# Kernel optimization log

Hardware: AMD Instinct MI355X
Metric: run time of the kernel (lower is better)

## Reference

```python
import jax, jax.numpy as jnp
import numpy as np

B, C, H, W = 32, 64, 32, 32
DIM = H * W          # number of tokens (pixels)
DEPTH = 8
TAU = 1.0
NUM_CLASSES = 10


def setup_inputs() -> dict:
    key = jax.random.key(0)
    ks = jax.random.split(key, 6)
    return {
        "image": jax.random.normal(ks[0], (B, C, H, W), dtype=jnp.float32),
        "WV": 10.0 * jax.random.normal(ks[1], (C, C), dtype=jnp.float32),
        "WK": jax.random.normal(ks[2], (C, C), dtype=jnp.float32),
        "WQ": jax.random.normal(ks[3], (C, C), dtype=jnp.float32),
        "last_W": jax.random.normal(ks[4], (NUM_CLASSES, DIM), dtype=jnp.float32) / np.sqrt(DIM),
        "last_b": jnp.zeros((NUM_CLASSES,), dtype=jnp.float32),
    }


def reference(image, WV, WK, WQ, last_W, last_b):
    # flatten(2).transpose(1,2): (B,C,H,W) -> (B, H*W, C)
    X = image.reshape(B, C, DIM).transpose(0, 2, 1)
    scale = DIM ** (-0.5)
    for _ in range(DEPTH):
        # weight_sharing=True, sign=0 -> W = WV every layer
        Q = X @ WQ                                  # (B, n, C)
        K = X @ WK                                  # (B, n, C)
        scores = jnp.einsum('bnc,bmc->bnm', Q, K) * scale  # (B, n, n)
        A = jax.nn.softmax(scores, axis=-1)
        # diffusion_step (method 'A'): tau * A @ (X @ W) + X
        X = TAU * jnp.einsum('bnm,bmc->bnc', A, X @ WV) + X
    # mean over channel dim -> (B, dim), then Linear(dim, num_classes)
    pred = X.mean(-1) @ last_W.T + last_b
    return pred
```

## Files before the change

### kernel.cpp

```cpp
#include <hip/hip_runtime.h>
#include <math.h>

#define BB    32
#define CCH   64
#define DIMN  1024
#define NCLS  10

typedef __attribute__((ext_vector_type(8))) short bf16x8;
typedef __attribute__((ext_vector_type(4))) float f32x4;
typedef __attribute__((ext_vector_type(4))) unsigned short us4;
typedef __attribute__((ext_vector_type(8))) unsigned short us8;

#define MFMA16(a, b, c) __builtin_amdgcn_mfma_f32_16x16x32_bf16(a, b, c, 0, 0, 0)

__device__ __forceinline__ unsigned short f2bf(float x) {
  unsigned u = __float_as_uint(x);
  unsigned r = u + 0x7fffu + ((u >> 16) & 1u);
  return (unsigned short)(r >> 16);
}
__device__ __forceinline__ float bf2f(unsigned short h) {
  return __uint_as_float(((unsigned)h) << 16);
}
__device__ __forceinline__ void split3_pk(float x0, float x1,
                                          unsigned& hp, unsigned& mp,
                                          unsigned& lp) {
  unsigned h, m, l;
  asm("v_cvt_pk_bf16_f32 %0, %1, %2" : "=v"(h) : "v"(x0), "v"(x1));
  const float h0 = __uint_as_float(h << 16);
  const float h1 = __uint_as_float(h & 0xffff0000u);
  const float r0 = x0 - h0, r1 = x1 - h1;
  asm("v_cvt_pk_bf16_f32 %0, %1, %2" : "=v"(m) : "v"(r0), "v"(r1));
  const float m0 = __uint_as_float(m << 16);
  const float m1 = __uint_as_float(m & 0xffff0000u);
  asm("v_cvt_pk_bf16_f32 %0, %1, %2" : "=v"(l) : "v"(r0 - m0), "v"(r1 - m1));
  hp = h; mp = m; lp = l;
}
__device__ __forceinline__ void split3_pk2(float x0, float x1,
    unsigned short& h0, unsigned short& m0, unsigned short& l0,
    unsigned short& h1, unsigned short& m1, unsigned short& l1) {
  unsigned h, m, l;
  split3_pk(x0, x1, h, m, l);
  h0 = (unsigned short)h; h1 = (unsigned short)(h >> 16);
  m0 = (unsigned short)m; m1 = (unsigned short)(m >> 16);
  l0 = (unsigned short)l; l1 = (unsigned short)(l >> 16);
}
__device__ __forceinline__ void split3_frag(const float* xv, bf16x8& fh,
                                            bf16x8& fm, bf16x8& fl) {
  union U { bf16x8 v; unsigned d[4]; } uh, um, ul;
  #pragma unroll
  for (int p = 0; p < 4; ++p)
    split3_pk(xv[2 * p], xv[2 * p + 1], uh.d[p], um.d[p], ul.d[p]);
  fh = uh.v; fm = um.v; fl = ul.v;
}
__device__ __forceinline__ bf16x8 ld16B(const unsigned short* p) {
  union { us8 u; bf16x8 v; } c;
  c.u = *(const us8*)p;
  return c.v;
}

__global__ __launch_bounds__(256) void k_transpose(const float* __restrict__ img,
                                                   float* __restrict__ X) {
  __shared__ float tile[64][65];
  const int b  = blockIdx.y;
  const int n0 = blockIdx.x * 64;
  const int tx = threadIdx.x & 63;
  const int ty = threadIdx.x >> 6;
  const float* src = img + (size_t)b * CCH * DIMN;
  #pragma unroll
  for (int c = ty; c < 64; c += 4)
    tile[c][tx] = src[(size_t)c * DIMN + n0 + tx];
  __syncthreads();
  float* dst = X + (size_t)b * DIMN * CCH;
  #pragma unroll
  for (int nn = ty; nn < 64; nn += 4)
    dst[(size_t)(n0 + nn) * CCH + tx] = tile[tx][nn];
}

__device__ __forceinline__ void qkv_inner(
    const float xs[16][64],
    const float* __restrict__ WQ, const float* __restrict__ WK,
    const float* __restrict__ WV, int c, int tg,
    float qa[4], float ka[4], float va[4]) {
  for (int j = 0; j < 64; j += 4) {
    float4 xv[4];
    #pragma unroll
    for (int r = 0; r < 4; ++r)
      xv[r] = *(const float4*)&xs[tg * 4 + r][j];
    #pragma unroll
    for (int jj = 0; jj < 4; ++jj) {
      const float wq = WQ[(j + jj) * 64 + c];
      const float wk = WK[(j + jj) * 64 + c];
      const float wv = WV[(j + jj) * 64 + c];
      #pragma unroll
      for (int r = 0; r < 4; ++r) {
        const float x = ((const float*)&xv[r])[jj];
        qa[r] = fmaf(x, wq, qa[r]);
        ka[r] = fmaf(x, wk, ka[r]);
        va[r] = fmaf(x, wv, va[r]);
      }
    }
  }
}

__global__ __launch_bounds__(256) void k_qkv_split(
    const float* __restrict__ X,
    const float* __restrict__ WQ, const float* __restrict__ WK,
    const float* __restrict__ WV,
    float* __restrict__ Q,
    unsigned short* __restrict__ Kh, unsigned short* __restrict__ Km,
    unsigned short* __restrict__ Kl,
    unsigned short* __restrict__ VhT, unsigned short* __restrict__ VmT,
    unsigned short* __restrict__ VlT) {
  __shared__ float xs[16][64];
  __shared__ unsigned short vs[3][16][64];
  const int c  = threadIdx.x & 63;
  const int tg = threadIdx.x >> 6;
  const size_t t0 = (size_t)blockIdx.x * 16;
  #pragma unroll
  for (int r = tg; r < 16; r += 4)
    xs[r][c] = X[(t0 + r) * 64 + c];
  __syncthreads();
  float qa[4] = {0.f,0.f,0.f,0.f};
  float ka[4] = {0.f,0.f,0.f,0.f};
  float va[4] = {0.f,0.f,0.f,0.f};
  qkv_inner(xs, WQ, WK, WV, c, tg, qa, ka, va);
  #pragma unroll
  for (int pr = 0; pr < 2; ++pr) {
    const int r0 = 2 * pr, r1 = 2 * pr + 1;
    const int ta = tg * 4 + r0, tb = tg * 4 + r1;
    const size_t ia = (t0 + ta) * 64 + c;
    const size_t ib = (t0 + tb) * 64 + c;
    Q[ia] = qa[r0]; Q[ib] = qa[r1];
    unsigned short h0, m0, l0, h1, m1, l1;
    split3_pk2(ka[r0], ka[r1], h0, m0, l0, h1, m1, l1);
    Kh[ia] = h0; Km[ia] = m0; Kl[ia] = l0;
    Kh[ib] = h1; Km[ib] = m1; Kl[ib] = l1;
    split3_pk2(va[r0], va[r1], h0, m0, l0, h1, m1, l1);
    vs[0][ta][c] = h0; vs[1][ta][c] = m0; vs[2][ta][c] = l0;
    vs[0][tb][c] = h1; vs[1][tb][c] = m1; vs[2][tb][c] = l1;
  }
  __syncthreads();
  {
    const int row  = threadIdx.x >> 2;
    const int part = threadIdx.x & 3;
    const size_t bofs = (t0 >> 10) * ((size_t)DIMN * 64);
    const size_t kt   = (t0 & 1023) >> 5;
    const size_t tin  = (size_t)part * 8 + ((t0 & 31) >> 2);
    unsigned short* dst[3] = {VhT, VmT, VlT};
    #pragma unroll
    for (int term = 0; term < 3; ++term) {
      us4 pk;
      #pragma unroll
      for (int i = 0; i < 4; ++i) pk[i] = vs[term][part * 4 + i][row];
      *(us4*)&dst[term][bofs + kt * 2048 + (size_t)row * 32 + tin] = pk;
    }
  }
}

__global__ __launch_bounds__(256) void k_qkv_merge(
    float* __restrict__ X,
    const float* __restrict__ Mp, const float* __restrict__ Lp,
    const float* __restrict__ Op,
    const float* __restrict__ WQ, const float* __restrict__ WK,
    const float* __restrict__ WV,
    float* __restrict__ Q,
    unsigned short* __restrict__ Kh, unsigned short* __restrict__ Km,
    unsigned short* __restrict__ Kl,
    unsigned short* __restrict__ VhT, unsigned short* __restrict__ VmT,
    unsigned short* __restrict__ VlT) {
  __shared__ float xs[16][64];
  __shared__ unsigned short vs[3][16][64];
  const int c  = threadIdx.x & 63;
  const int tg = threadIdx.x >> 6;
  const size_t t0 = (size_t)blockIdx.x * 16;
  #pragma unroll
  for (int r = tg; r < 16; r += 4) {
    const size_t grow = t0 + r;
    const float m0 = Mp[grow], m1 = Mp[32768 + grow];
    const float l0 = Lp[grow], l1 = Lp[32768 + grow];
    const float mm = fmaxf(m0, m1);
    const float w0 = __expf(m0 - mm), w1 = __expf(m1 - mm);
    const float inv = 1.0f / (l0 * w0 + l1 * w1);
    const float o0 = Op[grow * 64 + c];
    const float o1 = Op[(size_t)2097152 + grow * 64 + c];
    const float xn = X[grow * 64 + c] + (o0 * w0 + o1 * w1) * inv;
    X[grow * 64 + c] = xn;
    xs[r][c] = xn;
  }
  __syncthreads();
  float qa[4] = {0.f,0.f,0.f,0.f};
  float ka[4] = {0.f,0.f,0.f,0.f};
  float va[4] = {0.f,0.f,0.f,0.f};
  qkv_inner(xs, WQ, WK, WV, c, tg, qa, ka, va);
  #pragma unroll
  for (int pr = 0; pr < 2; ++pr) {
    const int r0 = 2 * pr, r1 = 2 * pr + 1;
    const int ta = tg * 4 + r0, tb = tg * 4 + r1;
    const size_t ia = (t0 + ta) * 64 + c;
    const size_t ib = (t0 + tb) * 64 + c;
    Q[ia] = qa[r0]; Q[ib] = qa[r1];
    unsigned short h0, m0, l0, h1, m1, l1;
    split3_pk2(ka[r0], ka[r1], h0, m0, l0, h1, m1, l1);
    Kh[ia] = h0; Km[ia] = m0; Kl[ia] = l0;
    Kh[ib] = h1; Km[ib] = m1; Kl[ib] = l1;
    split3_pk2(va[r0], va[r1], h0, m0, l0, h1, m1, l1);
    vs[0][ta][c] = h0; vs[1][ta][c] = m0; vs[2][ta][c] = l0;
    vs[0][tb][c] = h1; vs[1][tb][c] = m1; vs[2][tb][c] = l1;
  }
  __syncthreads();
  {
    const int row  = threadIdx.x >> 2;
    const int part = threadIdx.x & 3;
    const size_t bofs = (t0 >> 10) * ((size_t)DIMN * 64);
    const size_t kt   = (t0 & 1023) >> 5;
    const size_t tin  = (size_t)part * 8 + ((t0 & 31) >> 2);
    unsigned short* dst[3] = {VhT, VmT, VlT};
    #pragma unroll
    for (int term = 0; term < 3; ++term) {
      us4 pk;
      #pragma unroll
      for (int i = 0; i < 4; ++i) pk[i] = vs[term][part * 4 + i][row];
      *(us4*)&dst[term][bofs + kt * 2048 + (size_t)row * 32 + tin] = pk;
    }
  }
}

__global__ __launch_bounds__(256, 2) void k_attn_sk(
    const float* __restrict__ Qg,
    const unsigned short* __restrict__ Kh, const unsigned short* __restrict__ Km,
    const unsigned short* __restrict__ Kl,
    const unsigned short* __restrict__ VhT, const unsigned short* __restrict__ VmT,
    const unsigned short* __restrict__ VlT,
    float* __restrict__ Mp, float* __restrict__ Lp, float* __restrict__ Op) {
  __shared__ __align__(16) unsigned short Khs[32 * 72];
  __shared__ __align__(16) unsigned short Kms[32 * 72];
  __shared__ __align__(16) unsigned short Kls[32 * 72];
  __shared__ __align__(16) unsigned short Vhs[64 * 40];
  __shared__ __align__(16) unsigned short Vms[64 * 40];
  __shared__ __align__(16) unsigned short Vls[64 * 40];

  const int tid  = threadIdx.x;
  const int w    = tid >> 6;
  const int lane = tid & 63;
  const int ln   = lane & 15;
  const int q    = lane >> 4;

  const int bid   = blockIdx.x;
  const int xcd   = bid & 7;
  const int seq   = bid >> 3;
  const int b     = xcd * 4 + (seq >> 4);
  const int local = seq & 15;
  const int half  = local >> 3;
  const int i0    = (local & 7) * 128;

  const size_t base = (size_t)b * (DIMN * 64);
  const float scale = 0.03125f;

  const int kj = tid >> 3, kg = tid & 7;
  const int vc = tid >> 2, vg = tid & 3;
  const int klo = kj * 72 + kg * 8;
  const int vlo = vc * 40 + vg * 8;

  bf16x8 qh[2][2], qm[2][2], ql[2][2];
  #pragma unroll
  for (int t = 0; t < 2; ++t) {
    const int mrow = i0 + 64 * t + 16 * w + ln;
    const float* qp = Qg + base + (size_t)mrow * 64 + 8 * q;
    #pragma unroll
    for (int s = 0; s < 2; ++s) {
      const float4 x0 = ((const float4*)(qp + 32 * s))[0];
      const float4 x1 = ((const float4*)(qp + 32 * s))[1];
      const float xv[8] = {x0.x, x0.y, x0.z, x0.w, x1.x, x1.y, x1.z, x1.w};
      split3_frag(xv, qh[t][s], qm[t][s], ql[t][s]);
    }
  }

  f32x4 O[2][4];
  #pragma unroll
  for (int t = 0; t < 2; ++t)
    #pragma unroll
    for (int ct = 0; ct < 4; ++ct) O[t][ct] = (f32x4){0.f, 0.f, 0.f, 0.f};
  float m_run[2] = {-INFINITY, -INFINITY};
  float l_run[2] = {0.f, 0.f};

  const int kt0 = half * 16;
  for (int kt = kt0; kt < kt0 + 16; ++kt) {
    __syncthreads();

    {
      const size_t tof = base + (size_t)kt * 2048 + tid * 8;
      const us8 a0 = *(const us8*)&Kh[tof];
      const us8 a1 = *(const us8*)&Km[tof];
      const us8 a2 = *(const us8*)&Kl[tof];
      const us8 b0 = *(const us8*)&VhT[tof];
      const us8 b1 = *(const us8*)&VmT[tof];
      const us8 b2 = *(const us8*)&VlT[tof];
      *(us8*)&Khs[klo] = a0;
      *(us8*)&Kms[klo] = a1;
      *(us8*)&Kls[klo] = a2;
      *(us8*)&Vhs[vlo] = b0;
      *(us8*)&Vms[vlo] = b1;
      *(us8*)&Vls[vlo] = b2;
    }
    __syncthreads();

    f32x4 sacc[2][2];
    __builtin_amdgcn_s_setprio(1);
    #pragma unroll
    for (int ct = 0; ct < 2; ++ct) {
      f32x4 aA = (f32x4){0.f, 0.f, 0.f, 0.f};
      f32x4 aB = (f32x4){0.f, 0.f, 0.f, 0.f};
      #pragma unroll
      for (int s = 0; s < 2; ++s) {
        const int ko = (16 * ct + ln) * 72 + 32 * s + 8 * q;
        const bf16x8 bh = ld16B(&Khs[ko]);
        const bf16x8 bm = ld16B(&Kms[ko]);
        const bf16x8 bl = ld16B(&Kls[ko]);
        aA = MFMA16(bh, ql[0][s], aA);
        aA = MFMA16(bl, qh[0][s], aA);
        aA = MFMA16(bm, qm[0][s], aA);
        aA = MFMA16(bh, qm[0][s], aA);
        aA = MFMA16(bm, qh[0][s], aA);
        aA = MFMA16(bh, qh[0][s], aA);
        aB = MFMA16(bh, ql[1][s], aB);
        aB = MFMA16(bl, qh[1][s], aB);
        aB = MFMA16(bm, qm[1][s], aB);
        aB = MFMA16(bh, qm[1][s], aB);
        aB = MFMA16(bm, qh[1][s], aB);
        aB = MFMA16(bh, qh[1][s], aB);
      }
      sacc[0][ct] = aA; sacc[1][ct] = aB;
    }
    __builtin_amdgcn_s_setprio(0);

    bf16x8 ph[2], pm[2], pl[2];
    const int srcb = (lane & 48) + ((lane & 48) >> 2);
    #pragma unroll
    for (int t = 0; t < 2; ++t) {
      float m8 = fmaxf(fmaxf(fmaxf(sacc[t][0][0], sacc[t][0][1]),
                             fmaxf(sacc[t][0][2], sacc[t][0][3])),
                       fmaxf(fmaxf(sacc[t][1][0], sacc[t][1][1]),
                             fmaxf(sacc[t][1][2], sacc[t][1][3])));
      m8 = fmaxf(m8, __shfl_xor(m8, 16, 64));
      m8 = fmaxf(m8, __shfl_xor(m8, 32, 64));
      const float mnew  = fmaxf(m_run[t], m8 * scale);
      const float alpha = __expf(m_run[t] - mnew);
      m_run[t] = mnew;

      float pv[8];
      float s8 = 0.f;
      #pragma unroll
      for (int ct = 0; ct < 2; ++ct) {
        #pragma unroll
        for (int r = 0; r < 4; ++r) {
          const float p = __expf(sacc[t][ct][r] * scale - m_run[t]);
          pv[ct * 4 + r] = p;
          s8 += p;
        }
      }
      float sr = s8 + __shfl_xor(s8, 16, 64);
      sr = sr + __shfl_xor(sr, 32, 64);
      l_run[t] = l_run[t] * alpha + sr;

      float arow[4];
      #pragma unroll
      for (int r = 0; r < 4; ++r) arow[r] = __shfl(alpha, srcb + r, 64);
      #pragma unroll
      for (int ct = 0; ct < 4; ++ct) {
        #pragma unroll
        for (int r = 0; r < 4; ++r) O[t][ct][r] *= arow[r];
      }

      split3_frag(pv, ph[t], pm[t], pl[t]);
    }

    __builtin_amdgcn_s_setprio(1);
    #pragma unroll
    for (int ct = 0; ct < 4; ++ct) {
      const int vo = (16 * ct + ln) * 40 + 8 * q;
      const bf16x8 vvh = ld16B(&Vhs[vo]);
      const bf16x8 vvm = ld16B(&Vms[vo]);
      const bf16x8 vvl = ld16B(&Vls[vo]);
      O[0][ct] = MFMA16(ph[0], vvh, O[0][ct]);
      O[0][ct] = MFMA16(ph[0], vvm, O[0][ct]);
      O[0][ct] = MFMA16(pm[0], vvh, O[0][ct]);
      O[0][ct] = MFMA16(pm[0], vvm, O[0][ct]);
      O[0][ct] = MFMA16(ph[0], vvl, O[0][ct]);
      O[0][ct] = MFMA16(pl[0], vvh, O[0][ct]);
      O[1][ct] = MFMA16(ph[1], vvh, O[1][ct]);
      O[1][ct] = MFMA16(ph[1], vvm, O[1][ct]);
      O[1][ct] = MFMA16(pm[1], vvh, O[1][ct]);
      O[1][ct] = MFMA16(pm[1], vvm, O[1][ct]);
      O[1][ct] = MFMA16(ph[1], vvl, O[1][ct]);
      O[1][ct] = MFMA16(pl[1], vvh, O[1][ct]);
    }
    __builtin_amdgcn_s_setprio(0);
  }

  const size_t hofs = (size_t)half * (32 * 1024);
  #pragma unroll
  for (int t = 0; t < 2; ++t) {
    const int ti0 = i0 + 64 * t;
    #pragma unroll
    for (int r = 0; r < 4; ++r) {
      const int row = ti0 + 16 * w + 4 * q + r;
      const size_t grow = hofs + (size_t)b * DIMN + row;
      #pragma unroll
      for (int ct = 0; ct < 4; ++ct)
        Op[grow * 64 + ln + 16 * ct] = O[t][ct][r];
    }
    if (q == 0) {
      const size_t tgrow = hofs + (size_t)b * DIMN + ti0 + 16 * w + ln;
      Mp[tgrow] = m_run[t];
      Lp[tgrow] = l_run[t];
    }
  }
}

__global__ __launch_bounds__(256) void k_merge_mean(
    const float* __restrict__ X,
    const float* __restrict__ Mp, const float* __restrict__ Lp,
    const float* __restrict__ Op, float* __restrict__ meanv) {
  const int c  = threadIdx.x & 63;
  const int tg = threadIdx.x >> 6;
  const size_t t0 = (size_t)blockIdx.x * 128;
  for (int i = tg; i < 128; i += 4) {
    const size_t grow = t0 + i;
    const float m0 = Mp[grow], m1 = Mp[32768 + grow];
    const float l0 = Lp[grow], l1 = Lp[32768 + grow];
    const float mm = fmaxf(m0, m1);
    const float w0 = __expf(m0 - mm), w1 = __expf(m1 - mm);
    const float inv = 1.0f / (l0 * w0 + l1 * w1);
    const float o0 = Op[grow * 64 + c];
    const float o1 = Op[(size_t)2097152 + grow * 64 + c];
    float v = X[grow * 64 + c] + (o0 * w0 + o1 * w1) * inv;
    #pragma unroll
    for (int off = 32; off > 0; off >>= 1)
      v += __shfl_down(v, off, 64);
    if (c == 0) meanv[grow] = v * (1.0f / 64.0f);
  }
}

__global__ __launch_bounds__(256) void k_head2(
    const float* __restrict__ meanv, const float* __restrict__ lW,
    const float* __restrict__ lb, float* __restrict__ out) {
  __shared__ float red[256];
  const int b   = blockIdx.x;
  const int tid = threadIdx.x;
  float acc[NCLS];
  #pragma unroll
  for (int k = 0; k < NCLS; ++k) acc[k] = 0.f;
  for (int n = tid; n < DIMN; n += 256) {
    const float m = meanv[(size_t)b * DIMN + n];
    #pragma unroll
    for (int k = 0; k < NCLS; ++k)
      acc[k] = fmaf(m, lW[k * DIMN + n], acc[k]);
  }
  for (int k = 0; k < NCLS; ++k) {
    red[tid] = acc[k];
    __syncthreads();
    for (int s = 128; s > 0; s >>= 1) {
      if (tid < s) red[tid] += red[tid + s];
      __syncthreads();
    }
    if (tid == 0) out[b * NCLS + k] = red[0] + lb[k];
    __syncthreads();
  }
}

__global__ __launch_bounds__(256) void k_attn_s(
    const float* __restrict__ Qg,
    const unsigned short* __restrict__ Kh, const unsigned short* __restrict__ Km,
    const unsigned short* __restrict__ Kl,
    const unsigned short* __restrict__ VhT, const unsigned short* __restrict__ VmT,
    const unsigned short* __restrict__ VlT,
    float* __restrict__ X, float* __restrict__ meanout) {
  __shared__ __align__(16) unsigned short Khs[32 * 72];
  __shared__ __align__(16) unsigned short Kms[32 * 72];
  __shared__ __align__(16) unsigned short Kls[32 * 72];
  __shared__ __align__(16) unsigned short Vhs[64 * 40];
  __shared__ __align__(16) unsigned short Vms[64 * 40];
  __shared__ __align__(16) unsigned short Vls[64 * 40];

  const int tid  = threadIdx.x;
  const int w    = tid >> 6;
  const int lane = tid & 63;
  const int ln   = lane & 15;
  const int q    = lane >> 4;
  const int bid = blockIdx.x;
  const int xcd = bid & 7;
  const int seq = bid >> 3;
  const int b   = xcd * 4 + (seq >> 4);
  const int i0  = (seq & 15) * 64;
  const size_t base = (size_t)b * (DIMN * 64);
  const float scale = 0.03125f;

  const int kj = tid >> 3, kg = tid & 7;
  const int vc = tid >> 2, vg = tid & 3;
  const int klo = kj * 72 + kg * 8;
  const int vlo = vc * 40 + vg * 8;

  bf16x8 qh[2], qm[2], ql[2];
  {
    const int mrow = i0 + 16 * w + ln;
    const float* qp = Qg + base + (size_t)mrow * 64 + 8 * q;
    #pragma unroll
    for (int s = 0; s < 2; ++s) {
      const float4 x0 = ((const float4*)(qp + 32 * s))[0];
      const float4 x1 = ((const float4*)(qp + 32 * s))[1];
      const float xv[8] = {x0.x, x0.y, x0.z, x0.w, x1.x, x1.y, x1.z, x1.w};
      split3_frag(xv, qh[s], qm[s], ql[s]);
    }
  }

  f32x4 O[4];
  #pragma unroll
  for (int ct = 0; ct < 4; ++ct) O[ct] = (f32x4){0.f, 0.f, 0.f, 0.f};
  float m_run = -INFINITY;
  float l_run = 0.f;

  for (int kt = 0; kt < 32; ++kt) {
    __syncthreads();
    {
      const size_t tof = base + (size_t)kt * 2048 + tid * 8;
      const us8 a0 = *(const us8*)&Kh[tof];
      const us8 a1 = *(const us8*)&Km[tof];
      const us8 a2 = *(const us8*)&Kl[tof];
      const us8 b0 = *(const us8*)&VhT[tof];
      const us8 b1 = *(const us8*)&VmT[tof];
      const us8 b2 = *(const us8*)&VlT[tof];
      *(us8*)&Khs[klo] = a0;
      *(us8*)&Kms[klo] = a1;
      *(us8*)&Kls[klo] = a2;
      *(us8*)&Vhs[vlo] = b0;
      *(us8*)&Vms[vlo] = b1;
      *(us8*)&Vls[vlo] = b2;
    }
    __syncthreads();

    f32x4 sacc[2];
    #pragma unroll
    for (int ct = 0; ct < 2; ++ct) {
      f32x4 a = (f32x4){0.f, 0.f, 0.f, 0.f};
      #pragma unroll
      for (int s = 0; s < 2; ++s) {
        const int ko = (16 * ct + ln) * 72 + 32 * s + 8 * q;
        const bf16x8 bh = ld16B(&Khs[ko]);
        const bf16x8 bm = ld16B(&Kms[ko]);
        const bf16x8 bl = ld16B(&Kls[ko]);
        a = MFMA16(bh, ql[s], a);
        a = MFMA16(bl, qh[s], a);
        a = MFMA16(bm, qm[s], a);
        a = MFMA16(bh, qm[s], a);
        a = MFMA16(bm, qh[s], a);
        a = MFMA16(bh, qh[s], a);
      }
      sacc[ct] = a;
    }

    float m8 = fmaxf(fmaxf(fmaxf(sacc[0][0], sacc[0][1]),
                           fmaxf(sacc[0][2], sacc[0][3])),
                     fmaxf(fmaxf(sacc[1][0], sacc[1][1]),
                           fmaxf(sacc[1][2], sacc[1][3])));
    m8 = fmaxf(m8, __shfl_xor(m8, 16, 64));
    m8 = fmaxf(m8, __shfl_xor(m8, 32, 64));
    const float mnew  = fmaxf(m_run, m8 * scale);
    const float alpha = __expf(m_run - mnew);
    m_run = mnew;

    float pv[8];
    float s8 = 0.f;
    #pragma unroll
    for (int ct = 0; ct < 2; ++ct) {
      #pragma unroll
      for (int r = 0; r < 4; ++r) {
        const float p = __expf(sacc[ct][r] * scale - m_run);
        pv[ct * 4 + r] = p;
        s8 += p;
      }
    }
    float sr = s8 + __shfl_xor(s8, 16, 64);
    sr = sr + __shfl_xor(sr, 32, 64);
    l_run = l_run * alpha + sr;

    const int srcb = (lane & 48) + ((lane & 48) >> 2);
    float arow[4];
    #pragma unroll
    for (int r = 0; r < 4; ++r) arow[r] = __shfl(alpha, srcb + r, 64);
    #pragma unroll
    for (int ct = 0; ct < 4; ++ct) {
      #pragma unroll
      for (int r = 0; r < 4; ++r) O[ct][r] *= arow[r];
    }

    bf16x8 ph, pm, pl;
    split3_frag(pv, ph, pm, pl);

    #pragma unroll
    for (int ct = 0; ct < 4; ++ct) {
      const int vo = (16 * ct + ln) * 40 + 8 * q;
      const bf16x8 vvh = ld16B(&Vhs[vo]);
      const bf16x8 vvm = ld16B(&Vms[vo]);
      const bf16x8 vvl = ld16B(&Vls[vo]);
      O[ct] = MFMA16(ph, vvh, O[ct]);
      O[ct] = MFMA16(ph, vvm, O[ct]);
      O[ct] = MFMA16(pm, vvh, O[ct]);
      O[ct] = MFMA16(pm, vvm, O[ct]);
      O[ct] = MFMA16(ph, vvl, O[ct]);
      O[ct] = MFMA16(pl, vvh, O[ct]);
    }
  }

  const int srcb = (lane & 48) + ((lane & 48) >> 2);
  float linv[4];
  #pragma unroll
  for (int r = 0; r < 4; ++r) linv[r] = 1.0f / __shfl(l_run, srcb + r, 64);
  #pragma unroll
  for (int r = 0; r < 4; ++r) {
    const int row = i0 + 16 * w + 4 * q + r;
    float srow = 0.f;
    #pragma unroll
    for (int ct = 0; ct < 4; ++ct) {
      float* xp = X + base + (size_t)row * 64 + ln + 16 * ct;
      const float nv = *xp + O[ct][r] * linv[r];
      *xp = nv;
      srow += nv;
    }
    if (meanout) {
      #pragma unroll
      for (int mk = 1; mk <= 8; mk <<= 1)
        srow += __shfl_xor(srow, mk, 64);
      if (ln == 0) meanout[(size_t)b * DIMN + row] = srow * (1.0f / 64.0f);
    }
  }
}

extern "C" void kernel_launch(void* const* d_in, const int* in_sizes, int n_in,
                              void* d_out, int out_size, void* d_ws, size_t ws_size,
                              hipStream_t stream) {
  const float* image = (const float*)d_in[0];
  const float* WV    = (const float*)d_in[1];
  const float* WK    = (const float*)d_in[2];
  const float* WQ    = (const float*)d_in[3];
  const float* lW    = (const float*)d_in[4];
  const float* lb    = (const float*)d_in[5];
  float* out = (float*)d_out;

  float* ws = (float*)d_ws;
  const size_t NELEM = (size_t)BB * DIMN * CCH;
  const size_t NROW  = (size_t)BB * DIMN;

  const size_t need_sk   = (7 * NELEM + 5 * NROW) * sizeof(float);
  const size_t need_fast = (5 * NELEM + NROW) * sizeof(float);

  if (ws_size >= need_sk) {
    float* X = ws;
    float* Q = ws + NELEM;
    unsigned short* Kh  = (unsigned short*)(ws + 2 * NELEM);
    unsigned short* Km  = Kh + NELEM;
    unsigned short* Kl  = Kh + 2 * NELEM;
    unsigned short* VhT = Kh + 3 * NELEM;
    unsigned short* VmT = Kh + 4 * NELEM;
    unsigned short* VlT = Kh + 5 * NELEM;
    float* Op    = ws + 5 * NELEM;
    float* Mp    = ws + 7 * NELEM;
    float* Lp    = Mp + 2 * NROW;
    float* meanv = Lp + 2 * NROW;

    k_transpose<<<dim3(DIMN / 64, BB), 256, 0, stream>>>(image, X);
    k_qkv_split<<<(BB * DIMN) / 16, 256, 0, stream>>>(
        X, WQ, WK, WV, Q, Kh, Km, Kl, VhT, VmT, VlT);
    for (int layer = 0; layer < 8; ++layer) {
      k_attn_sk<<<512, 256, 0, stream>>>(
          Q, Kh, Km, Kl, VhT, VmT, VlT, Mp, Lp, Op);
      if (layer < 7)
        k_qkv_merge<<<(BB * DIMN) / 16, 256, 0, stream>>>(
            X, Mp, Lp, Op, WQ, WK, WV, Q, Kh, Km, Kl, VhT, VmT, VlT);
    }
    k_merge_mean<<<256, 256, 0, stream>>>(X, Mp, Lp, Op, meanv);
    k_head2<<<BB, 256, 0, stream>>>(meanv, lW, lb, out);
  } else {
    float* X = ws;
    float* Q = ws + NELEM;
    unsigned short* Kh  = (unsigned short*)(ws + 2 * NELEM);
    unsigned short* Km  = Kh + NELEM;
    unsigned short* Kl  = Kh + 2 * NELEM;
    unsigned short* VhT = Kh + 3 * NELEM;
    unsigned short* VmT = Kh + 4 * NELEM;
    unsigned short* VlT = Kh + 5 * NELEM;
    float* meanv = ws + 5 * NELEM;
    (void)need_fast;

    k_transpose<<<dim3(DIMN / 64, BB), 256, 0, stream>>>(image, X);
    for (int layer = 0; layer < 8; ++layer) {
      k_qkv_split<<<(BB * DIMN) / 16, 256, 0, stream>>>(
          X, WQ, WK, WV, Q, Kh, Km, Kl, VhT, VmT, VlT);
      k_attn_s<<<512, 256, 0, stream>>>(
          Q, Kh, Km, Kl, VhT, VmT, VlT, X, (layer == 7) ? meanv : nullptr);
    }
    k_head2<<<BB, 256, 0, stream>>>(meanv, lW, lb, out);
  }
}
```

Before: 700.9 us.

## Double-buffer K/V tiles in LDS with register prefetch in attention kernel

The attention kernel now keeps two LDS buffers for the K and V hi/mid/lo tiles. It issues the global loads for the next tile into registers before the MFMA compute on the current tile and writes them to the other buffer afterwards. This lets global memory latency overlap with compute and removes one barrier per iteration. LDS use doubles to about 58KB per block, which may limit the two-blocks-per-CU target, and the held registers raise register pressure.

Result: faster. 676.7 us (-3.4%).

```diff
diff --git a/kernel.cpp b/kernel.cpp
--- a/kernel.cpp
+++ b/kernel.cpp
@@ -232,12 +232,7 @@
     const unsigned short* __restrict__ VhT, const unsigned short* __restrict__ VmT,
     const unsigned short* __restrict__ VlT,
     float* __restrict__ Mp, float* __restrict__ Lp, float* __restrict__ Op) {
-  __shared__ __align__(16) unsigned short Khs[32 * 72];
-  __shared__ __align__(16) unsigned short Kms[32 * 72];
-  __shared__ __align__(16) unsigned short Kls[32 * 72];
-  __shared__ __align__(16) unsigned short Vhs[64 * 40];
-  __shared__ __align__(16) unsigned short Vms[64 * 40];
-  __shared__ __align__(16) unsigned short Vls[64 * 40];
+  __shared__ __align__(16) unsigned short lds[2][14592];
 
   const int tid  = threadIdx.x;
   const int w    = tid >> 6;
@@ -284,25 +279,47 @@
   float l_run[2] = {0.f, 0.f};
 
   const int kt0 = half * 16;
+
+  {
+    const size_t tof = base + (size_t)kt0 * 2048 + tid * 8;
+    const us8 a0 = *(const us8*)&Kh[tof];
+    const us8 a1 = *(const us8*)&Km[tof];
+    const us8 a2 = *(const us8*)&Kl[tof];
+    const us8 b0 = *(const us8*)&VhT[tof];
+    const us8 b1 = *(const us8*)&VmT[tof];
+    const us8 b2 = *(const us8*)&VlT[tof];
+    unsigned short* B = lds[0];
+    *(us8*)&B[klo]          = a0;
+    *(us8*)&B[2304  + klo]  = a1;
+    *(us8*)&B[4608  + klo]  = a2;
+    *(us8*)&B[6912  + vlo]  = b0;
+    *(us8*)&B[9472  + vlo]  = b1;
+    *(us8*)&B[12032 + vlo]  = b2;
+  }
+
+  us8 ra0, ra1, ra2, rb0, rb1, rb2;
+
   for (int kt = kt0; kt < kt0 + 16; ++kt) {
+    const int cur = (kt - kt0) & 1;
     __syncthreads();
 
-    {
-      const size_t tof = base + (size_t)kt * 2048 + tid * 8;
-      const us8 a0 = *(const us8*)&Kh[tof];
-      const us8 a1 = *(const us8*)&Km[tof];
-      const us8 a2 = *(const us8*)&Kl[tof];
-      const us8 b0 = *(const us8*)&VhT[tof];
-      const us8 b1 = *(const us8*)&VmT[tof];
-      const us8 b2 = *(const us8*)&VlT[tof];
-      *(us8*)&Khs[klo] = a0;
-      *(us8*)&Kms[klo] = a1;
-      *(us8*)&Kls[klo] = a2;
-      *(us8*)&Vhs[vlo] = b0;
-      *(us8*)&Vms[vlo] = b1;
-      *(us8*)&Vls[vlo] = b2;
-    }
-    __syncthreads();
+    const bool have_next = (kt + 1 < kt0 + 16);
+    if (have_next) {
+      const size_t tof = base + (size_t)(kt + 1) * 2048 + tid * 8;
+      ra0 = *(const us8*)&Kh[tof];
+      ra1 = *(const us8*)&Km[tof];
+      ra2 = *(const us8*)&Kl[tof];
+      rb0 = *(const us8*)&VhT[tof];
+      rb1 = *(const us8*)&VmT[tof];
+      rb2 = *(const us8*)&VlT[tof];
+    }
+
+    const unsigned short* Khs = lds[cur];
+    const unsigned short* Kms = lds[cur] + 2304;
+    const unsigned short* Kls = lds[cur] + 4608;
+    const unsigned short* Vhs = lds[cur] + 6912;
+    const unsigned short* Vms = lds[cur] + 9472;
+    const unsigned short* Vls = lds[cur] + 12032;
 
     f32x4 sacc[2][2];
     __builtin_amdgcn_s_setprio(1);
@@ -395,6 +412,16 @@
       O[1][ct] = MFMA16(pl[1], vvh, O[1][ct]);
     }
     __builtin_amdgcn_s_setprio(0);
+
+    if (have_next) {
+      unsigned short* N = lds[cur ^ 1];
+      *(us8*)&N[klo]          = ra0;
+      *(us8*)&N[2304  + klo]  = ra1;
+      *(us8*)&N[4608  + klo]  = ra2;
+      *(us8*)&N[6912  + vlo]  = rb0;
+      *(us8*)&N[9472  + vlo]  = rb1;
+      *(us8*)&N[12032 + vlo]  = rb2;
+    }
   }
 
   const size_t hofs = (size_t)half * (32 * 1024);
```
